# Performance work log

Measured on AMD Instinct MI355X. Metric: run time of the kernel, lower is better.

Reference implementation:

```python
import jax, jax.numpy as jnp
import numpy as np

B, S, H = 16, 4096, 512   # batch, seq frames, conv_dim[-1]
G, V, D = 2, 320, 256     # groups, codevectors per group, codevector_dim


def setup_inputs() -> dict:
    key = jax.random.key(0)
    k1, k2, k3 = jax.random.split(key, 3)
    hidden_states = jax.random.normal(k1, (B, S, H), dtype=jnp.float32)
    W = jax.random.normal(k2, (H, G * V), dtype=jnp.float32) * 0.02
    b = jnp.zeros((G * V,), dtype=jnp.float32)
    codevectors = jax.random.normal(k3, (1, G * V, D // G), dtype=jnp.float32)
    return {"hidden_states": hidden_states, "W": W, "b": b,
            "codevectors": codevectors, "num_groups": G}


def reference(hidden_states, W, b, codevectors, num_groups):
    Bb, Ss, Hh = hidden_states.shape
    GV = W.shape[1]
    g = num_groups
    v = GV // g
    d = codevectors.shape[-1]
    BT = Bb * Ss

    # weight_proj: [B,S,H] @ [H, G*V] -> logits per (token, group, var)
    logits = (hidden_states @ W + b).reshape(BT, g, v)

    # eval path: hard argmax one-hot over codevectors per group
    idx = jnp.argmax(logits, axis=-1)              # [BT, g] int

    # one-hot x codebook multiply-reduce == gather from codebook
    cb = codevectors.reshape(g, v, d)              # [g, v, d]
    gathered = cb[jnp.arange(g)[None, :], idx]     # [BT, g, d]
    out = gathered.reshape(Bb, Ss, g * d)          # [B, S, codevector_dim]

    # perplexity over one-hot probs: marginal = mean of one-hots = counts/BT
    marginal = jnp.zeros((g, v), dtype=jnp.float32)
    marginal = marginal.at[jnp.arange(g)[None, :], idx].add(1.0) / BT
    perplexity = jnp.exp(-jnp.sum(marginal * jnp.log(marginal + 1e-7), axis=-1)).sum()

    return out, perplexity
```

## Files before the change

kernel.cpp:

```cpp
#include <hip/hip_runtime.h>
#include <hip/hip_bf16.h>
#include <hip/hip_fp8.h>

constexpr int BT = 65536;
constexpr int K  = 512;
constexpr int V  = 320;
constexpr int G  = 2;
constexpr int Dg = 128;
constexpr int MT = 64;
constexpr int NSTEP = 8;
constexpr size_t WS_IMG = 4096;

using f32x4 = __attribute__((ext_vector_type(4))) float;

static __device__ __forceinline__ unsigned cvt4(float a, float b, float c, float d) {
#if __has_builtin(__builtin_amdgcn_cvt_pk_fp8_f32)
    int r = 0;
    r = __builtin_amdgcn_cvt_pk_fp8_f32(a, b, r, false);
    r = __builtin_amdgcn_cvt_pk_fp8_f32(c, d, r, true);
    return (unsigned)r;
#else
    __hip_fp8_e4m3 ha(a), hb(b), hc(c), hd(d);
    return (unsigned)ha.__x | ((unsigned)hb.__x << 8) |
           ((unsigned)hc.__x << 16) | ((unsigned)hd.__x << 24);
#endif
}
static __device__ __forceinline__ long long mk64(unsigned lo, unsigned hi) {
    return (long long)(((unsigned long long)hi << 32) | lo);
}
static __device__ __forceinline__ f32x4 mfma_fp8(long long a, long long b, f32x4 c) {
    return __builtin_amdgcn_mfma_f32_16x16x32_fp8_fp8(a, b, c, 0, 0, 0);
}

__global__ __launch_bounds__(256) void vq_prep(const float* __restrict__ Wm,
                                               unsigned char* __restrict__ img)
{
    int id   = blockIdx.x * 256 + threadIdx.x;
    int lane = id & 63;
    int r    = id >> 6;
    int nt   = r % 5;  r /= 5;
    int wc   = r & 3;  r >>= 2;
    int s    = r & 7;
    int g    = r >> 3;
    int col  = g * V + wc * 80 + nt * 16 + (lane & 15);
    int kb   = s * 64 + (lane >> 4) * 8;
    float v0[8], v1[8];
#pragma unroll
    for (int j = 0; j < 8; ++j) {
        v0[j] = 16.0f * Wm[(size_t)(kb + j) * 640 + col];
        v1[j] = 16.0f * Wm[(size_t)(kb + 32 + j) * 640 + col];
    }
    *reinterpret_cast<uint4*>(img + (size_t)id * 16) =
        make_uint4(cvt4(v0[0], v0[1], v0[2], v0[3]), cvt4(v0[4], v0[5], v0[6], v0[7]),
                   cvt4(v1[0], v1[1], v1[2], v1[3]), cvt4(v1[4], v1[5], v1[6], v1[7]));
}

__global__ __launch_bounds__(512) void vq_main(
    const float* __restrict__ hs, const unsigned char* __restrict__ img,
    const float* __restrict__ bv, const float* __restrict__ cbv,
    float* __restrict__ out, unsigned int* __restrict__ hist)
{
    __shared__ __align__(16) unsigned char smem[24576];

    const int tid  = threadIdx.x;
    const int bid  = blockIdx.x;
    const int g    = (bid >> 3) & 1;
    const int rblk = (bid & 7) | ((bid >> 4) << 3);
    const int r0   = rblk * MT;
    const int w    = tid >> 6;
    const int lane = tid & 63;
    const int l4   = lane & 15;
    const int wc   = w & 3;
    const int h    = w >> 2;

    f32x4 acc[2][5] = {};

    const int arow = tid >> 3, akq = tid & 7;
    const float* aptr = hs + (size_t)(r0 + arow) * K + akq * 8;
    const int awoff = (arow >> 4) * 1024 + ((arow & 15) + 16 * (akq & 3)) * 16 + (akq >> 2) * 8;
    const int a_rd0 = (h * 2 + 0) * 1024 + lane * 16;
    const int a_rd1 = (h * 2 + 1) * 1024 + lane * 16;
    const unsigned char* bsrc = img + (size_t)g * 163840 + (size_t)tid * 16;
    const int b_rd = 4096 + wc * 5 * 1024 + lane * 16;

    auto packA = [&](float4 x, float4 y) {
        *reinterpret_cast<uint2*>(&smem[awoff]) =
            make_uint2(cvt4(x.x, x.y, x.z, x.w), cvt4(y.x, y.y, y.z, y.w));
    };

    float4 ax = *reinterpret_cast<const float4*>(aptr);
    float4 ay = *reinterpret_cast<const float4*>(aptr + 4);

    for (int s = 0; s < NSTEP; ++s) {
        const unsigned char* bs = bsrc + (size_t)s * 20480;
#pragma unroll
        for (int i = 0; i < 2; ++i)
            __builtin_amdgcn_global_load_lds(
                (const __attribute__((address_space(1))) void*)(bs + i * 8192),
                (__attribute__((address_space(3))) void*)(&smem[4096 + i * 8192 + tid * 16]),
                16, 0, 0);
        if (tid < 256)
            __builtin_amdgcn_global_load_lds(
                (const __attribute__((address_space(1))) void*)(bs + 16384),
                (__attribute__((address_space(3))) void*)(&smem[4096 + 16384 + tid * 16]),
                16, 0, 0);
        packA(ax, ay);
        __syncthreads();
        if (s + 1 < NSTEP) {
            ax = *reinterpret_cast<const float4*>(aptr + (s + 1) * 64);
            ay = *reinterpret_cast<const float4*>(aptr + (s + 1) * 64 + 4);
        }
        __builtin_amdgcn_s_setprio(1);
        {
            uint4 a0 = *reinterpret_cast<const uint4*>(&smem[a_rd0]);
            uint4 a1 = *reinterpret_cast<const uint4*>(&smem[a_rd1]);
            long long a0k0 = mk64(a0.x, a0.y), a0k1 = mk64(a0.z, a0.w);
            long long a1k0 = mk64(a1.x, a1.y), a1k1 = mk64(a1.z, a1.w);
#pragma unroll
            for (int nt = 0; nt < 5; ++nt) {
                uint4 bb = *reinterpret_cast<const uint4*>(&smem[b_rd + nt * 1024]);
                long long bk0 = mk64(bb.x, bb.y), bk1 = mk64(bb.z, bb.w);
                acc[0][nt] = mfma_fp8(a0k0, bk0, acc[0][nt]);
                acc[0][nt] = mfma_fp8(a0k1, bk1, acc[0][nt]);
                acc[1][nt] = mfma_fp8(a1k0, bk0, acc[1][nt]);
                acc[1][nt] = mfma_fp8(a1k1, bk1, acc[1][nt]);
            }
        }
        __builtin_amdgcn_s_setprio(0);
        __syncthreads();
    }

    float biasv[5];
#pragma unroll
    for (int nt = 0; nt < 5; ++nt) biasv[nt] = 16.0f * bv[g * V + wc * 80 + nt * 16 + l4];

    float* red_v = reinterpret_cast<float*>(smem);
    int*   red_i = reinterpret_cast<int*>(smem + 1024);
    int*   idx_s = reinterpret_cast<int*>(smem + 2048);

#pragma unroll
    for (int mt = 0; mt < 2; ++mt) {
#pragma unroll
        for (int reg = 0; reg < 4; ++reg) {
            float bestv = acc[mt][0][reg] + biasv[0];
            int   besti = wc * 80 + l4;
#pragma unroll
            for (int nt = 1; nt < 5; ++nt) {
                float v = acc[mt][nt][reg] + biasv[nt];
                int   ci = wc * 80 + nt * 16 + l4;
                if (v > bestv) { bestv = v; besti = ci; }
            }
#pragma unroll
            for (int m = 1; m < 16; m <<= 1) {
                float ov = __shfl_xor(bestv, m);
                int   oi = __shfl_xor(besti, m);
                if (ov > bestv || (ov == bestv && oi < besti)) { bestv = ov; besti = oi; }
            }
            if (l4 == 0) {
                int row = h * 32 + mt * 16 + (lane >> 4) * 4 + reg;
                red_v[row * 4 + wc] = bestv;
                red_i[row * 4 + wc] = besti;
            }
        }
    }
    __syncthreads();

    int my_bi = -1;
    if (tid < MT) {
        float bb = red_v[tid * 4]; int bi = red_i[tid * 4];
#pragma unroll
        for (int c = 1; c < 4; ++c) {
            float v = red_v[tid * 4 + c]; int ii = red_i[tid * 4 + c];
            if (v > bb || (v == bb && ii < bi)) { bb = v; bi = ii; }
        }
        idx_s[tid] = bi;
        my_bi = bi;
    }
    __syncthreads();

#pragma unroll
    for (int i = 0; i < 4; ++i) {
        int idx = i * 512 + tid;
        int row = idx >> 5;
        int d4  = idx & 31;
        int vi  = idx_s[row];
        float4 val = *reinterpret_cast<const float4*>(&cbv[((size_t)(g * V + vi)) * Dg + d4 * 4]);
        *reinterpret_cast<float4*>(&out[((size_t)(r0 + row)) * (G * Dg) + g * Dg + d4 * 4]) = val;
    }
    if (my_bi >= 0) atomicAdd(&hist[g * V + my_bi], 1u);
}

__global__ void vq_ppl(const unsigned int* __restrict__ hist, float* __restrict__ outp)
{
    int lane = threadIdx.x;
    float ppl = 0.0f;
    for (int g = 0; g < G; ++g) {
        float local = 0.0f;
        for (int v = lane; v < V; v += 64) {
            float m = (float)hist[g * V + v] * (1.0f / (float)BT);
            local += m * logf(m + 1e-7f);
        }
#pragma unroll
        for (int off = 32; off; off >>= 1) local += __shfl_down(local, off);
        if (lane == 0) ppl += expf(-local);
    }
    if (lane == 0) outp[0] = ppl;
}

extern "C" void kernel_launch(void* const* d_in, const int* in_sizes, int n_in,
                              void* d_out, int out_size, void* d_ws, size_t ws_size,
                              hipStream_t stream)
{
    const float* hs  = (const float*)d_in[0];
    const float* Wm  = (const float*)d_in[1];
    const float* bv  = (const float*)d_in[2];
    const float* cbv = (const float*)d_in[3];
    float* out = (float*)d_out;

    unsigned int*  hist = (unsigned int*)d_ws;
    unsigned char* img  = (unsigned char*)d_ws + WS_IMG;

    hipMemsetAsync(d_ws, 0, G * V * sizeof(unsigned int), stream);
    vq_prep<<<80, 256, 0, stream>>>(Wm, img);
    vq_main<<<2048, 512, 0, stream>>>(hs, img, bv, cbv, out, hist);
    vq_ppl<<<1, 64, 0, stream>>>(hist, out + (size_t)BT * G * Dg);
}
```

Baseline: 85.02 us.

## Load B fragments directly from global and double-buffer A tile in LDS

Each wave now reads its pre-packed fp8 weight fragments straight from global memory (expected to hit in L2) rather than staging them through LDS with global_load_lds. The activation tile is double-buffered in LDS with a two-step register prefetch, so each k-step needs only one barrier where it previously needed two. LDS use drops from 24 KB to 8 KB, which may allow more resident blocks. The trade-off is global load latency directly on the MFMA path and higher register pressure from the fully unrolled loop.

```diff
diff --git a/kernel.cpp b/kernel.cpp
--- a/kernel.cpp
+++ b/kernel.cpp
@@ -60,7 +60,7 @@
     const float* __restrict__ bv, const float* __restrict__ cbv,
     float* __restrict__ out, unsigned int* __restrict__ hist)
 {
-    __shared__ __align__(16) unsigned char smem[24576];
+    __shared__ __align__(16) unsigned char smem[8192];
 
     const int tid  = threadIdx.x;
     const int bid  = blockIdx.x;
@@ -80,46 +80,45 @@
     const int awoff = (arow >> 4) * 1024 + ((arow & 15) + 16 * (akq & 3)) * 16 + (akq >> 2) * 8;
     const int a_rd0 = (h * 2 + 0) * 1024 + lane * 16;
     const int a_rd1 = (h * 2 + 1) * 1024 + lane * 16;
-    const unsigned char* bsrc = img + (size_t)g * 163840 + (size_t)tid * 16;
-    const int b_rd = 4096 + wc * 5 * 1024 + lane * 16;
-
-    auto packA = [&](float4 x, float4 y) {
-        *reinterpret_cast<uint2*>(&smem[awoff]) =
+    const unsigned char* bwv = img + (size_t)g * 163840 + wc * 5120 + (size_t)lane * 16;
+
+    auto packA = [&](float4 x, float4 y, int sel) {
+        *reinterpret_cast<uint2*>(&smem[sel * 4096 + awoff]) =
             make_uint2(cvt4(x.x, x.y, x.z, x.w), cvt4(y.x, y.y, y.z, y.w));
     };
 
-    float4 ax = *reinterpret_cast<const float4*>(aptr);
-    float4 ay = *reinterpret_cast<const float4*>(aptr + 4);
-
+    float4 aX[2], aY[2];
+    aX[0] = *reinterpret_cast<const float4*>(aptr);
+    aY[0] = *reinterpret_cast<const float4*>(aptr + 4);
+    packA(aX[0], aY[0], 0);
+    aX[1] = *reinterpret_cast<const float4*>(aptr + 64);
+    aY[1] = *reinterpret_cast<const float4*>(aptr + 64 + 4);
+    __syncthreads();
+
+#pragma unroll
     for (int s = 0; s < NSTEP; ++s) {
-        const unsigned char* bs = bsrc + (size_t)s * 20480;
-#pragma unroll
-        for (int i = 0; i < 2; ++i)
-            __builtin_amdgcn_global_load_lds(
-                (const __attribute__((address_space(1))) void*)(bs + i * 8192),
-                (__attribute__((address_space(3))) void*)(&smem[4096 + i * 8192 + tid * 16]),
-                16, 0, 0);
-        if (tid < 256)
-            __builtin_amdgcn_global_load_lds(
-                (const __attribute__((address_space(1))) void*)(bs + 16384),
-                (__attribute__((address_space(3))) void*)(&smem[4096 + 16384 + tid * 16]),
-                16, 0, 0);
-        packA(ax, ay);
-        __syncthreads();
-        if (s + 1 < NSTEP) {
-            ax = *reinterpret_cast<const float4*>(aptr + (s + 1) * 64);
-            ay = *reinterpret_cast<const float4*>(aptr + (s + 1) * 64 + 4);
-        }
+        const int cur = s & 1, nxt = cur ^ 1;
+        if (s + 1 < NSTEP) packA(aX[nxt], aY[nxt], nxt);
+        if (s + 2 < NSTEP) {
+            aX[cur] = *reinterpret_cast<const float4*>(aptr + (s + 2) * 64);
+            aY[cur] = *reinterpret_cast<const float4*>(aptr + (s + 2) * 64 + 4);
+        }
+        const unsigned char* bs = bwv + (size_t)s * 20480;
         __builtin_amdgcn_s_setprio(1);
         {
-            uint4 a0 = *reinterpret_cast<const uint4*>(&smem[a_rd0]);
-            uint4 a1 = *reinterpret_cast<const uint4*>(&smem[a_rd1]);
+            uint4 b0 = *reinterpret_cast<const uint4*>(bs);
+            uint4 b1 = *reinterpret_cast<const uint4*>(bs + 1024);
+            uint4 b2 = *reinterpret_cast<const uint4*>(bs + 2048);
+            uint4 b3 = *reinterpret_cast<const uint4*>(bs + 3072);
+            uint4 b4 = *reinterpret_cast<const uint4*>(bs + 4096);
+            uint4 a0 = *reinterpret_cast<const uint4*>(&smem[cur * 4096 + a_rd0]);
+            uint4 a1 = *reinterpret_cast<const uint4*>(&smem[cur * 4096 + a_rd1]);
             long long a0k0 = mk64(a0.x, a0.y), a0k1 = mk64(a0.z, a0.w);
             long long a1k0 = mk64(a1.x, a1.y), a1k1 = mk64(a1.z, a1.w);
+            uint4 bb[5] = {b0, b1, b2, b3, b4};
 #pragma unroll
             for (int nt = 0; nt < 5; ++nt) {
-                uint4 bb = *reinterpret_cast<const uint4*>(&smem[b_rd + nt * 1024]);
-                long long bk0 = mk64(bb.x, bb.y), bk1 = mk64(bb.z, bb.w);
+                long long bk0 = mk64(bb[nt].x, bb[nt].y), bk1 = mk64(bb[nt].z, bb[nt].w);
                 acc[0][nt] = mfma_fp8(a0k0, bk0, acc[0][nt]);
                 acc[0][nt] = mfma_fp8(a0k1, bk1, acc[0][nt]);
                 acc[1][nt] = mfma_fp8(a1k0, bk0, acc[1][nt]);
```

Result: slower. 88.60 us (+4.2%).
